# Kernel optimization log

Measured on AMD Instinct MI355X. Metric: run time of the kernel, lower is better.

Reference implementation:

```python
import jax, jax.numpy as jnp
import numpy as np
from jax import lax

DIM = 256
HEADS = 8
B, H, W = 8, 128, 128
EPS_LN = 1e-5
EPS_NORM = 1e-12


def _ln(x, w, b):
    # WithBias LayerNorm over channel dim, x: [b,c,h,w]
    mu = x.mean(axis=1, keepdims=True)
    var = ((x - mu) ** 2).mean(axis=1, keepdims=True)
    return (x - mu) / jnp.sqrt(var + EPS_LN) * w[None, :, None, None] + b[None, :, None, None]


def _conv1x1(x, w, b):
    # w: [out,in]
    return jnp.einsum('bchw,oc->bohw', x, w) + b[None, :, None, None]


def _dwconv3(x, w, b=None):
    # depthwise 3x3, w: [C,1,3,3]
    c = x.shape[1]
    y = lax.conv_general_dilated(x, w, (1, 1), 'SAME',
                                 dimension_numbers=('NCHW', 'OIHW', 'NCHW'),
                                 feature_group_count=c)
    if b is not None:
        y = y + b[None, :, None, None]
    return y


def setup_inputs() -> dict:
    key = jax.random.key(0)
    ks = jax.random.split(key, 10)
    s = 0.02
    return {
        'x': jax.random.normal(ks[0], (B, DIM, H, W), jnp.float32),
        'hx': jax.random.normal(ks[1], (B, DIM, H, W), jnp.float32),
        'ln1_w': jnp.ones((DIM,), jnp.float32),
        'ln1_b': jnp.zeros((DIM,), jnp.float32),
        'ln2_w': jnp.ones((DIM,), jnp.float32),
        'ln2_b': jnp.zeros((DIM,), jnp.float32),
        'q_w': jax.random.normal(ks[2], (DIM, DIM), jnp.float32) * s,
        'q_b': jnp.zeros((DIM,), jnp.float32),
        'q_dw_w': jax.random.normal(ks[3], (DIM, 1, 3, 3), jnp.float32) * s,
        'q_dw_b': jnp.zeros((DIM,), jnp.float32),
        'kv_w': jax.random.normal(ks[4], (2 * DIM, DIM), jnp.float32) * s,
        'kv_b': jnp.zeros((2 * DIM,), jnp.float32),
        'kv_dw_w': jax.random.normal(ks[5], (2 * DIM, 1, 3, 3), jnp.float32) * s,
        'kv_dw_b': jnp.zeros((2 * DIM,), jnp.float32),
        'ao_w': jax.random.normal(ks[6], (DIM, DIM), jnp.float32) * s,
        'ao_b': jnp.zeros((DIM,), jnp.float32),
        'pe1_w': jax.random.normal(ks[7], (DIM, 1, 3, 3), jnp.float32) * s,
        'pe2_w': jax.random.normal(ks[8], (DIM, 1, 3, 3), jnp.float32) * s,
        'temperature': jnp.ones((HEADS, 1, 1), jnp.float32),
    }


def reference(x, hx, ln1_w, ln1_b, ln2_w, ln2_b, q_w, q_b, q_dw_w, q_dw_b,
              kv_w, kv_b, kv_dw_w, kv_dw_b, ao_w, ao_b, pe1_w, pe2_w, temperature):
    b, c, h, w = hx.shape
    q = _dwconv3(_conv1x1(_ln(x, ln1_w, ln1_b), q_w, q_b), q_dw_w, q_dw_b)
    kv = _dwconv3(_conv1x1(_ln(hx, ln2_w, ln2_b), kv_w, kv_b), kv_dw_w, kv_dw_b)
    k, v = jnp.split(kv, 2, axis=1)
    # positional embedding branch: dwconv -> GELU -> dwconv (no bias)
    p_emb = _dwconv3(jax.nn.gelu(_dwconv3(v, pe1_w)), pe2_w)
    hd = c // HEADS
    # [b, head, hd, hw]
    qh = q.reshape(b, HEADS, hd, h * w)
    kh = k.reshape(b, HEADS, hd, h * w)
    vh = v.reshape(b, HEADS, hd, h * w)
    qh = qh / jnp.maximum(jnp.linalg.norm(qh, axis=-1, keepdims=True), EPS_NORM)
    kh = kh / jnp.maximum(jnp.linalg.norm(kh, axis=-1, keepdims=True), EPS_NORM)
    attn = jnp.einsum('bhcn,bhdn->bhcd', qh, kh) * temperature[None]
    attn = jax.nn.softmax(attn, axis=-1)
    out = jnp.einsum('bhcd,bhdn->bhcn', attn, vh).reshape(b, c, h, w)
    return _conv1x1(out, ao_w, ao_b) + p_emb + hx
```

## Files before the change

kernel.cpp:

```cpp
#include <hip/hip_runtime.h>
#include <cstdio>
#include <cstdint>

typedef unsigned short u16;
typedef short short8 __attribute__((ext_vector_type(8)));
typedef float floatx4 __attribute__((ext_vector_type(4)));

#define NPIX 16384
#define DIM 256

__device__ inline float bf2f(u16 v) {
    return __uint_as_float(((uint32_t)v) << 16);
}
__device__ inline u16 f2bf(float f) {
    uint32_t u = __float_as_uint(f);
    u += 0x7fffu + ((u >> 16) & 1u);
    return (u16)(u >> 16);
}
__device__ inline float gelu_fast(float x) {
    float x3 = x * x * x;
    float z2 = 1.5957691216057308f * (x + 0.044715f * x3);
    return x * __builtin_amdgcn_rcpf(1.f + __expf(-z2));
}
__device__ inline void load8(const u16* p, size_t idx, int isf32, float out[8]) {
    if (isf32) {
        const float4* f = (const float4*)((const float*)p + idx);
        float4 a = f[0], b = f[1];
        out[0] = a.x; out[1] = a.y; out[2] = a.z; out[3] = a.w;
        out[4] = b.x; out[5] = b.y; out[6] = b.z; out[7] = b.w;
    } else {
        uint4 d = *(const uint4*)(p + idx);
        u16 v[8]; *(uint4*)v = d;
#pragma unroll
        for (int j = 0; j < 8; ++j) out[j] = bf2f(v[j]);
    }
}

__global__ __launch_bounds__(256)
void detect_dtype(const u16* __restrict__ x, int* __restrict__ flag) {
    __shared__ int sh[256];
    int t = threadIdx.x;
    const uint32_t* w = (const uint32_t*)x;
    int cnt = 0;
    for (int i = t; i < 4096; i += 256) {
        int e = (w[i] >> 7) & 0xFF;
        if (e >= 110 && e <= 134) cnt++;
    }
    sh[t] = cnt;
    __syncthreads();
    if (t == 0) {
        int s = 0;
        for (int i = 0; i < 256; ++i) s += sh[i];
        *flag = (s < 2048) ? 1 : 0;
    }
}

struct WArgs {
    const void* src[17];
    int off[17];
    int n[17];
};
__global__ __launch_bounds__(256)
void convert_params(WArgs a, const int* __restrict__ flag, u16* __restrict__ dst) {
    int isf32 = *flag;
    int w = blockIdx.y;
    const void* s = a.src[w];
    u16* d = dst + a.off[w];
    int n = a.n[w];
    for (int i = blockIdx.x * 256 + threadIdx.x; i < n; i += gridDim.x * 256)
        d[i] = isf32 ? f2bf(((const float*)s)[i]) : ((const u16*)s)[i];
}

__global__ __launch_bounds__(256)
void ln_stats(const u16* __restrict__ x, const int* __restrict__ flag,
              float* __restrict__ mu, float* __restrict__ rstd) {
    int isf32 = *flag;
    int g = blockIdx.x * 256 + threadIdx.x;
    int b = g >> 14, n = g & (NPIX - 1);
    float s = 0.f, s2 = 0.f;
    if (isf32) {
        const float* p = (const float*)x + (size_t)b * DIM * NPIX + n;
        for (int c = 0; c < DIM; ++c) { float v = p[(size_t)c * NPIX]; s += v; s2 += v * v; }
    } else {
        const u16* p = x + (size_t)b * DIM * NPIX + n;
        for (int c = 0; c < DIM; ++c) { float v = bf2f(p[(size_t)c * NPIX]); s += v; s2 += v * v; }
    }
    float m = s * (1.f / 256.f);
    float var = s2 * (1.f / 256.f) - m * m;
    mu[g] = m;
    rstd[g] = rsqrtf(var + 1e-5f);
}

__global__ __launch_bounds__(256)
void ln_transpose(const u16* __restrict__ x, const int* __restrict__ flag,
                  const float* __restrict__ mu, const float* __restrict__ rstd,
                  const u16* __restrict__ lnw, const u16* __restrict__ lnb,
                  u16* __restrict__ xt) {
    int isf32 = *flag;
    __shared__ u16 T[64][72];
    int b = blockIdx.x >> 8;
    int n0 = (blockIdx.x & 255) * 64;
    int c0 = blockIdx.y * 64;
    int t = threadIdx.x;
#pragma unroll
    for (int l = 0; l < 2; ++l) {
        int idx = t + l * 256;
        int cl = idx >> 3, nch = (idx & 7) * 8;
        float vals[8];
        load8(x, ((size_t)(b * DIM + c0 + cl)) * NPIX + n0 + nch, isf32, vals);
        float w = bf2f(lnw[c0 + cl]), bb = bf2f(lnb[c0 + cl]);
#pragma unroll
        for (int j = 0; j < 8; ++j) {
            int g = b * NPIX + n0 + nch + j;
            float v = (vals[j] - mu[g]) * rstd[g] * w + bb;
            T[nch + j][cl] = f2bf(v);
        }
    }
    __syncthreads();
#pragma unroll
    for (int l = 0; l < 2; ++l) {
        int idx = t + l * 256;
        int nl = idx >> 3, cch = (idx & 7) * 8;
        uint4 d = *(const uint4*)&T[nl][cch];
        *(uint4*)(xt + (size_t)(b * NPIX + n0 + nl) * DIM + c0 + cch) = d;
    }
}

template <int HAS_ADD>
__global__ __launch_bounds__(256)
void gemm_bf16(const u16* __restrict__ A, const u16* __restrict__ Bw,
               const u16* __restrict__ bias, const u16* __restrict__ addt,
               u16* __restrict__ C, int ldc) {
    __shared__ u16 As[128][40];
    __shared__ u16 Bs[128][40];
    const int m0 = blockIdx.x * 128;
    const int n0 = blockIdx.y * 128;
    const int t = threadIdx.x;
    const int lane = t & 63;
    const int wid = t >> 6;
    const int wm = (wid >> 1) * 64;
    const int wn = (wid & 1) * 64;
    const int frow = lane & 15;
    const int koff = (lane >> 4) * 8;
    floatx4 acc[4][4] = {};
    for (int k0 = 0; k0 < 256; k0 += 32) {
#pragma unroll
        for (int l = 0; l < 2; ++l) {
            int idx = t + l * 256;
            int r = idx >> 2, ch = (idx & 3) * 8;
            *(uint4*)&As[r][ch] = *(const uint4*)(A + (size_t)(m0 + r) * 256 + k0 + ch);
            *(uint4*)&Bs[r][ch] = *(const uint4*)(Bw + (size_t)(n0 + r) * 256 + k0 + ch);
        }
        __syncthreads();
        short8 af[4], bfr[4];
#pragma unroll
        for (int i = 0; i < 4; ++i) {
            af[i] = *(const short8*)&As[wm + i * 16 + frow][koff];
            bfr[i] = *(const short8*)&Bs[wn + i * 16 + frow][koff];
        }
#pragma unroll
        for (int i = 0; i < 4; ++i)
#pragma unroll
            for (int j = 0; j < 4; ++j)
                acc[i][j] = __builtin_amdgcn_mfma_f32_16x16x32_bf16(af[i], bfr[j], acc[i][j], 0, 0, 0);
        __syncthreads();
    }
    const int col = lane & 15;
    const int r0 = (lane >> 4) * 4;
#pragma unroll
    for (int j = 0; j < 4; ++j) {
        int o = n0 + wn + j * 16 + col;
        float bv = bf2f(bias[o]);
#pragma unroll
        for (int i = 0; i < 4; ++i) {
#pragma unroll
            for (int r = 0; r < 4; ++r) {
                int m = m0 + wm + i * 16 + r0 + r;
                size_t off = (size_t)m * ldc + o;
                float v = acc[i][j][r] + bv;
                if (HAS_ADD) v += bf2f(addt[off]);
                C[off] = f2bf(v);
            }
        }
    }
}

template <int C, int HAS_BIAS, int DO_GELU>
__global__ __launch_bounds__(256)
void dwconv3_reg(const u16* __restrict__ in, int in_stride, int in_off,
                 const u16* __restrict__ w9, const u16* __restrict__ bias,
                 u16* __restrict__ out, int out_stride, int out_off) {
    constexpr int TPP = C / 8;
    constexpr int GRP = 256 / TPP;
    constexpr int XSEG = 128 / (GRP * 4);
    int t = threadIdx.x;
    int cl = t & (TPP - 1);
    int g = t / TPP;
    int c8 = cl * 8;
    int blk = blockIdx.x;
    int xs = blk & (XSEG - 1);
    int tmp = blk / XSEG;
    int y = tmp & 127;
    int b = tmp >> 7;
    int x0 = xs * (GRP * 4) + g * 4;

    u16 wl[72];
#pragma unroll
    for (int i = 0; i < 9; ++i)
        *((uint4*)wl + i) = *((const uint4*)(w9 + c8 * 9) + i);
    float wgt[9][8];
#pragma unroll
    for (int tap = 0; tap < 9; ++tap)
#pragma unroll
        for (int j = 0; j < 8; ++j)
            wgt[tap][j] = bf2f(wl[j * 9 + tap]);

    float acc[4][8] = {};
#pragma unroll
    for (int dy = -1; dy <= 1; ++dy) {
        int yy = y + dy;
        if ((unsigned)yy >= 128u) continue;
        const u16* rp = in + (size_t)(b * NPIX + yy * 128) * in_stride + in_off + c8;
#pragma unroll
        for (int ci = 0; ci < 6; ++ci) {
            int cc = x0 - 1 + ci;
            if ((unsigned)cc >= 128u) continue;
            uint4 d = *(const uint4*)(rp + (size_t)cc * in_stride);
            u16 v[8]; *(uint4*)v = d;
            float fv[8];
#pragma unroll
            for (int j = 0; j < 8; ++j) fv[j] = bf2f(v[j]);
#pragma unroll
            for (int dx = -1; dx <= 1; ++dx) {
                int p = ci - 1 - dx;
                if (p < 0 || p > 3) continue;
                int tap = (dy + 1) * 3 + (dx + 1);
#pragma unroll
                for (int j = 0; j < 8; ++j) acc[p][j] += fv[j] * wgt[tap][j];
            }
        }
    }

    float bi[8];
    if (HAS_BIAS) {
        uint4 bd = *(const uint4*)(bias + c8);
        u16 bv[8]; *(uint4*)bv = bd;
#pragma unroll
        for (int j = 0; j < 8; ++j) bi[j] = bf2f(bv[j]);
    }
    u16* op = out + (size_t)(b * NPIX + y * 128 + x0) * out_stride + out_off + c8;
#pragma unroll
    for (int p = 0; p < 4; ++p) {
        u16 o[8];
#pragma unroll
        for (int j = 0; j < 8; ++j) {
            float r = acc[p][j];
            if (HAS_BIAS) r += bi[j];
            if (DO_GELU) r = gelu_fast(r);
            o[j] = f2bf(r);
        }
        *(uint4*)(op + (size_t)p * out_stride) = *(uint4*)o;
    }
}

__global__ __launch_bounds__(256)
void finalize_scales(const float* __restrict__ qss, const float* __restrict__ kss,
                     float* __restrict__ qsc, float* __restrict__ ksc) {
    int i = blockIdx.x * 256 + threadIdx.x;
    qsc[i] = 1.f / fmaxf(sqrtf(qss[i]), 1e-12f);
    ksc[i] = 1.f / fmaxf(sqrtf(kss[i]), 1e-12f);
}

__global__ __launch_bounds__(256)
void gram_kernel(const u16* __restrict__ qT, const u16* __restrict__ kvT,
                 float* __restrict__ Gpart, float* __restrict__ qss,
                 float* __restrict__ kss) {
    int blk = blockIdx.x;
    int b = blk >> 7, chunk = blk & 127;
    int t = threadIdx.x;
    int hbase = t & 0xE0;
    int row0 = b * NPIX + chunk * 128;
    const u16* qp = qT + (size_t)row0 * 256 + t;
    const u16* kp = kvT + (size_t)row0 * 512;
    float acc[32];
#pragma unroll
    for (int j = 0; j < 32; ++j) acc[j] = 0.f;
    float qs2 = 0.f, ks2 = 0.f;
#pragma unroll 2
    for (int r = 0; r < 128; ++r) {
        float qv = bf2f(qp[(size_t)r * 256]);
        const u16* krow = kp + (size_t)r * 512;
        float kt = bf2f(krow[t]);
        qs2 += qv * qv;
        ks2 += kt * kt;
        uint4 k0 = *(const uint4*)(krow + hbase);
        uint4 k1 = *(const uint4*)(krow + hbase + 8);
        uint4 k2 = *(const uint4*)(krow + hbase + 16);
        uint4 k3 = *(const uint4*)(krow + hbase + 24);
        u16 kv16[32];
        *(uint4*)(kv16 + 0)  = k0;
        *(uint4*)(kv16 + 8)  = k1;
        *(uint4*)(kv16 + 16) = k2;
        *(uint4*)(kv16 + 24) = k3;
#pragma unroll
        for (int j = 0; j < 32; ++j) acc[j] += qv * bf2f(kv16[j]);
    }
    float* gp = Gpart + (size_t)blk * 8192 + t * 32;
#pragma unroll
    for (int j = 0; j < 32; j += 4)
        *(float4*)(gp + j) = make_float4(acc[j], acc[j + 1], acc[j + 2], acc[j + 3]);
    atomicAdd(&qss[b * 256 + t], qs2);
    atomicAdd(&kss[b * 256 + t], ks2);
}

__global__ __launch_bounds__(1024)
void softmax32(const float* __restrict__ Gpart, const float* __restrict__ qsc,
               const float* __restrict__ ksc, const u16* __restrict__ temp,
               float* __restrict__ attn) {
    int bh = blockIdx.x;
    int b = bh >> 3, h = bh & 7;
    int t = threadIdx.x;
    int i = t >> 5, j = t & 31;
    const float* gp = Gpart + (size_t)b * 128 * 8192 + (size_t)((h * 32 + i) * 32 + j);
    float s0 = 0.f, s1 = 0.f, s2 = 0.f, s3 = 0.f;
    for (int p = 0; p < 128; p += 4) {
        s0 += gp[(size_t)p * 8192];
        s1 += gp[(size_t)(p + 1) * 8192];
        s2 += gp[(size_t)(p + 2) * 8192];
        s3 += gp[(size_t)(p + 3) * 8192];
    }
    float qs = qsc[b * 256 + h * 32 + i];
    float ks = ksc[b * 256 + h * 32 + j];
    float tm = bf2f(temp[h]);
    float v = ((s0 + s1) + (s2 + s3)) * qs * ks * tm;
    float m = v;
    for (int s = 16; s; s >>= 1) m = fmaxf(m, __shfl_xor(m, s, 32));
    float e = __expf(v - m);
    float sum = e;
    for (int s = 16; s; s >>= 1) sum += __shfl_xor(sum, s, 32);
    attn[((size_t)(b * 8 + h) * 32 + i) * 32 + j] = e / sum;
}

__global__ __launch_bounds__(256)
void attnv_kernel(const float* __restrict__ attn, const u16* __restrict__ kvT,
                  u16* __restrict__ outT) {
    int blk = blockIdx.x;
    int b = blk >> 8, chunk = blk & 255;
    int t = threadIdx.x;
    int hbase = t & 0xE0;
    float at[32];
    const float4* ap = (const float4*)(attn + (size_t)b * 8192 + (size_t)t * 32);
#pragma unroll
    for (int j = 0; j < 8; ++j) {
        float4 d = ap[j];
        at[j * 4 + 0] = d.x; at[j * 4 + 1] = d.y;
        at[j * 4 + 2] = d.z; at[j * 4 + 3] = d.w;
    }
    int row0 = b * NPIX + chunk * 64;
    const u16* vp = kvT + (size_t)row0 * 512 + 256 + hbase;
    u16* op = outT + (size_t)row0 * 256 + t;
#pragma unroll 2
    for (int r = 0; r < 64; ++r) {
        const u16* vrow = vp + (size_t)r * 512;
        uint4 k0 = *(const uint4*)(vrow);
        uint4 k1 = *(const uint4*)(vrow + 8);
        uint4 k2 = *(const uint4*)(vrow + 16);
        uint4 k3 = *(const uint4*)(vrow + 24);
        u16 v16[32];
        *(uint4*)(v16 + 0)  = k0;
        *(uint4*)(v16 + 8)  = k1;
        *(uint4*)(v16 + 16) = k2;
        *(uint4*)(v16 + 24) = k3;
        float a = 0.f;
#pragma unroll
        for (int j = 0; j < 32; ++j) a += at[j] * bf2f(v16[j]);
        op[(size_t)r * 256] = f2bf(a);
    }
}

__global__ __launch_bounds__(256)
void final_out(const u16* __restrict__ Fp, const u16* __restrict__ hx,
               const int* __restrict__ flag, u16* __restrict__ out) {
    int isf32 = *flag;
    __shared__ u16 T[64][72];
    int b = blockIdx.x >> 8;
    int n0 = (blockIdx.x & 255) * 64;
    int c0 = blockIdx.y * 64;
    int t = threadIdx.x;
#pragma unroll
    for (int l = 0; l < 2; ++l) {
        int idx = t + l * 256;
        int nl = idx >> 3, cch = (idx & 7) * 8;
        *(uint4*)&T[nl][cch] = *(const uint4*)(Fp + (size_t)(b * NPIX + n0 + nl) * 256 + c0 + cch);
    }
    __syncthreads();
#pragma unroll
    for (int l = 0; l < 2; ++l) {
        int idx = t + l * 256;
        int cl = idx >> 3, nch = (idx & 7) * 8;
        size_t g = (size_t)(b * DIM + c0 + cl) * NPIX + n0 + nch;
        float hv[8];
        load8(hx, g, isf32, hv);
        float r[8];
#pragma unroll
        for (int j = 0; j < 8; ++j) r[j] = bf2f(T[nch + j][cl]) + hv[j];
        if (isf32) {
            float* o = (float*)out + g;
            *(float4*)o       = make_float4(r[0], r[1], r[2], r[3]);
            *(float4*)(o + 4) = make_float4(r[4], r[5], r[6], r[7]);
        } else {
            u16 ov[8];
#pragma unroll
            for (int j = 0; j < 8; ++j) ov[j] = f2bf(r[j]);
            *(uint4*)(out + g) = *(uint4*)ov;
        }
    }
}

__global__ void ws_marker(u16* out) {
    if (threadIdx.x < 64) ((uint32_t*)out)[threadIdx.x] = 0x46402400u;
}

extern "C" void kernel_launch(void* const* d_in, const int* in_sizes, int n_in,
                              void* d_out, int out_size, void* d_ws, size_t ws_size,
                              hipStream_t stream) {
    const u16* x    = (const u16*)d_in[0];
    const u16* hx   = (const u16*)d_in[1];
    u16* outp = (u16*)d_out;

    char* ws = (char*)d_ws;
    float* F = (float*)ws;
    float* mu_x   = F;
    float* rstd_x = F + 131072;
    float* mu_h   = F + 262144;
    float* rstd_h = F + 393216;
    float* qss    = F + 524288;
    float* kss    = F + 526336;
    float* qsc    = F + 528384;
    float* ksc    = F + 530432;
    float* attn   = F + 598016;
    int*   dflag  = (int*)(F + 663552);
    u16*   W      = (u16*)(ws + 2752512);
    u16* R1 = (u16*)(ws + (((size_t)4)   << 20));
    u16* R2 = (u16*)(ws + (((size_t)68)  << 20));
    u16* R3 = (u16*)(ws + (((size_t)132) << 20));
    u16* R4 = (u16*)(ws + (((size_t)260) << 20));
    float* Gpart = (float*)R2;

    size_t need = ((size_t)388) << 20;
    if (ws_size < need) {
        ws_marker<<<1, 64, 0, stream>>>(outp);
        return;
    }

    const int O_QW = 0, O_KVW = 65536, O_AOW = 196608, O_QB = 262144, O_KVB = 262400,
              O_AOB = 262912, O_LN1W = 263168, O_LN1B = 263424, O_LN2W = 263680,
              O_LN2B = 263936, O_QDWW = 264192, O_QDWB = 266496, O_KVDWW = 266752,
              O_KVDWB = 271360, O_PE1 = 271872, O_PE2 = 274176, O_TEMP = 276480;

    WArgs wa;
    const int srcidx[17] = {6, 10, 14, 7, 11, 15, 2, 3, 4, 5, 8, 9, 12, 13, 16, 17, 18};
    const int offs[17]   = {O_QW, O_KVW, O_AOW, O_QB, O_KVB, O_AOB, O_LN1W, O_LN1B,
                            O_LN2W, O_LN2B, O_QDWW, O_QDWB, O_KVDWW, O_KVDWB,
                            O_PE1, O_PE2, O_TEMP};
    const int ns[17]     = {65536, 131072, 65536, 256, 512, 256, 256, 256, 256, 256,
                            2304, 256, 4608, 512, 2304, 2304, 8};
    for (int i = 0; i < 17; ++i) { wa.src[i] = d_in[srcidx[i]]; wa.off[i] = offs[i]; wa.n[i] = ns[i]; }

    detect_dtype<<<1, 256, 0, stream>>>(x, dflag);
    convert_params<<<dim3(16, 17), 256, 0, stream>>>(wa, dflag, W);

    hipMemsetAsync(ws + (size_t)524288 * 4, 0, (size_t)(532480 - 524288) * 4, stream);

    ln_stats<<<512, 256, 0, stream>>>(x, dflag, mu_x, rstd_x);
    ln_stats<<<512, 256, 0, stream>>>(hx, dflag, mu_h, rstd_h);

    ln_transpose<<<dim3(2048, 4), 256, 0, stream>>>(x, dflag, mu_x, rstd_x, W + O_LN1W, W + O_LN1B, R1);
    gemm_bf16<0><<<dim3(1024, 2), 256, 0, stream>>>(R1, W + O_QW, W + O_QB, nullptr, R2, 256);

    ln_transpose<<<dim3(2048, 4), 256, 0, stream>>>(hx, dflag, mu_h, rstd_h, W + O_LN2W, W + O_LN2B, R1);
    gemm_bf16<0><<<dim3(1024, 4), 256, 0, stream>>>(R1, W + O_KVW, W + O_KVB, nullptr, R3, 512);

    dwconv3_reg<256, 1, 0><<<4096, 256, 0, stream>>>(R2, 256, 0, W + O_QDWW, W + O_QDWB, R1, 256, 0);
    dwconv3_reg<512, 1, 0><<<8192, 256, 0, stream>>>(R3, 512, 0, W + O_KVDWW, W + O_KVDWB, R4, 512, 0);

    gram_kernel<<<1024, 256, 0, stream>>>(R1, R4, Gpart, qss, kss);
    finalize_scales<<<8, 256, 0, stream>>>(qss, kss, qsc, ksc);
    softmax32<<<64, 1024, 0, stream>>>(Gpart, qsc, ksc, W + O_TEMP, attn);
    attnv_kernel<<<2048, 256, 0, stream>>>(attn, R4, R2);

    dwconv3_reg<256, 0, 1><<<4096, 256, 0, stream>>>(R4, 512, 256, W + O_PE1, nullptr, R3, 256, 0);
    dwconv3_reg<256, 0, 0><<<4096, 256, 0, stream>>>(R3, 256, 0, W + O_PE2, nullptr, R1, 256, 0);

    gemm_bf16<1><<<dim3(1024, 2), 256, 0, stream>>>(R2, W + O_AOW, W + O_AOB, R1, R3, 256);
    final_out<<<dim3(2048, 4), 256, 0, stream>>>(R3, hx, dflag, outp);
}
```

Baseline: 1.257 ms.

## Fuse LayerNorm stats with transpose, split gram into more chunks, inline norm scales

```diff
diff --git a/kernel.cpp b/kernel.cpp
--- a/kernel.cpp
+++ b/kernel.cpp
@@ -72,58 +72,70 @@
 }
 
 __global__ __launch_bounds__(256)
-void ln_stats(const u16* __restrict__ x, const int* __restrict__ flag,
-              float* __restrict__ mu, float* __restrict__ rstd) {
+void ln_fused(const u16* __restrict__ x, const int* __restrict__ flag,
+              const u16* __restrict__ lnw, const u16* __restrict__ lnb,
+              u16* __restrict__ xt) {
     int isf32 = *flag;
-    int g = blockIdx.x * 256 + threadIdx.x;
-    int b = g >> 14, n = g & (NPIX - 1);
+    __shared__ float T[32][257];
+    __shared__ float wsh[256], bsh[256];
+    __shared__ float2 red[8][32];
+    __shared__ float2 mst[32];
+    int t = threadIdx.x;
+    int b = blockIdx.x >> 9;
+    int n0 = (blockIdx.x & 511) * 32;
+    if (isf32) {
+        const float* xp = (const float*)x;
+#pragma unroll
+        for (int pass = 0; pass < 8; ++pass) {
+            int c = (t >> 3) + pass * 32;
+            int px = (t & 7) * 4;
+            float4 d = *(const float4*)(xp + ((size_t)(b * 256 + c)) * NPIX + n0 + px);
+            T[px][c] = d.x; T[px + 1][c] = d.y; T[px + 2][c] = d.z; T[px + 3][c] = d.w;
+        }
+    } else {
+#pragma unroll
+        for (int pass = 0; pass < 4; ++pass) {
+            int c = (t >> 2) + pass * 64;
+            int px = (t & 3) * 8;
+            uint4 d = *(const uint4*)(x + ((size_t)(b * 256 + c)) * NPIX + n0 + px);
+            u16 v[8]; *(uint4*)v = d;
+#pragma unroll
+            for (int j = 0; j < 8; ++j) T[px + j][c] = bf2f(v[j]);
+        }
+    }
+    wsh[t] = bf2f(lnw[t]);
+    bsh[t] = bf2f(lnb[t]);
+    __syncthreads();
+    int p = t & 31, q = t >> 5;
     float s = 0.f, s2 = 0.f;
-    if (isf32) {
-        const float* p = (const float*)x + (size_t)b * DIM * NPIX + n;
-        for (int c = 0; c < DIM; ++c) { float v = p[(size_t)c * NPIX]; s += v; s2 += v * v; }
-    } else {
-        const u16* p = x + (size_t)b * DIM * NPIX + n;
-        for (int c = 0; c < DIM; ++c) { float v = bf2f(p[(size_t)c * NPIX]); s += v; s2 += v * v; }
-    }
-    float m = s * (1.f / 256.f);
-    float var = s2 * (1.f / 256.f) - m * m;
-    mu[g] = m;
-    rstd[g] = rsqrtf(var + 1e-5f);
-}
-
-__global__ __launch_bounds__(256)
-void ln_transpose(const u16* __restrict__ x, const int* __restrict__ flag,
-                  const float* __restrict__ mu, const float* __restrict__ rstd,
-                  const u16* __restrict__ lnw, const u16* __restrict__ lnb,
-                  u16* __restrict__ xt) {
-    int isf32 = *flag;
-    __shared__ u16 T[64][72];
-    int b = blockIdx.x >> 8;
-    int n0 = (blockIdx.x & 255) * 64;
-    int c0 = blockIdx.y * 64;
-    int t = threadIdx.x;
-#pragma unroll
-    for (int l = 0; l < 2; ++l) {
-        int idx = t + l * 256;
-        int cl = idx >> 3, nch = (idx & 7) * 8;
-        float vals[8];
-        load8(x, ((size_t)(b * DIM + c0 + cl)) * NPIX + n0 + nch, isf32, vals);
-        float w = bf2f(lnw[c0 + cl]), bb = bf2f(lnb[c0 + cl]);
-#pragma unroll
-        for (int j = 0; j < 8; ++j) {
-            int g = b * NPIX + n0 + nch + j;
-            float v = (vals[j] - mu[g]) * rstd[g] * w + bb;
-            T[nch + j][cl] = f2bf(v);
-        }
-    }
+#pragma unroll
+    for (int k = 0; k < 32; ++k) {
+        float v = T[p][q * 32 + k];
+        s += v; s2 += v * v;
+    }
+    red[q][p] = make_float2(s, s2);
     __syncthreads();
-#pragma unroll
-    for (int l = 0; l < 2; ++l) {
-        int idx = t + l * 256;
-        int nl = idx >> 3, cch = (idx & 7) * 8;
-        uint4 d = *(const uint4*)&T[nl][cch];
-        *(uint4*)(xt + (size_t)(b * NPIX + n0 + nl) * DIM + c0 + cch) = d;
-    }
+    if (t < 32) {
+        float ss = 0.f, ss2 = 0.f;
+#pragma unroll
+        for (int qq = 0; qq < 8; ++qq) { ss += red[qq][t].x; ss2 += red[qq][t].y; }
+        float m = ss * (1.f / 256.f);
+        float var = ss2 * (1.f / 256.f) - m * m;
+        mst[t] = make_float2(m, rsqrtf(var + 1e-5f));
+    }
+    __syncthreads();
+    float2 ms = mst[p];
+    u16 ov[32];
+#pragma unroll
+    for (int k = 0; k < 32; ++k) {
+        int c = q * 32 + k;
+        float v = (T[p][c] - ms.x) * ms.y * wsh[c] + bsh[c];
+        ov[k] = f2bf(v);
+    }
+    u16* op = xt + ((size_t)(b * NPIX + n0 + p)) * 256 + q * 32;
+#pragma unroll
+    for (int k = 0; k < 32; k += 8)
+        *(uint4*)(op + k) = *(uint4*)(ov + k);
 }
 
 template <int HAS_ADD>
@@ -264,22 +276,14 @@
 }
 
 __global__ __launch_bounds__(256)
-void finalize_scales(const float* __restrict__ qss, const float* __restrict__ kss,
-                     float* __restrict__ qsc, float* __restrict__ ksc) {
-    int i = blockIdx.x * 256 + threadIdx.x;
-    qsc[i] = 1.f / fmaxf(sqrtf(qss[i]), 1e-12f);
-    ksc[i] = 1.f / fmaxf(sqrtf(kss[i]), 1e-12f);
-}
-
-__global__ __launch_bounds__(256)
 void gram_kernel(const u16* __restrict__ qT, const u16* __restrict__ kvT,
                  float* __restrict__ Gpart, float* __restrict__ qss,
                  float* __restrict__ kss) {
     int blk = blockIdx.x;
-    int b = blk >> 7, chunk = blk & 127;
+    int b = blk >> 8, chunk = blk & 255;
     int t = threadIdx.x;
     int hbase = t & 0xE0;
-    int row0 = b * NPIX + chunk * 128;
+    int row0 = b * NPIX + chunk * 64;
     const u16* qp = qT + (size_t)row0 * 256 + t;
     const u16* kp = kvT + (size_t)row0 * 512;
     float acc[32];
@@ -287,7 +291,7 @@
     for (int j = 0; j < 32; ++j) acc[j] = 0.f;
     float qs2 = 0.f, ks2 = 0.f;
 #pragma unroll 2
-    for (int r = 0; r < 128; ++r) {
+    for (int r = 0; r < 64; ++r) {
         float qv = bf2f(qp[(size_t)r * 256]);
         const u16* krow = kp + (size_t)r * 512;
         float kt = bf2f(krow[t]);
@@ -314,23 +318,23 @@
 }
 
 __global__ __launch_bounds__(1024)
-void softmax32(const float* __restrict__ Gpart, const float* __restrict__ qsc,
-               const float* __restrict__ ksc, const u16* __restrict__ temp,
+void softmax32(const float* __restrict__ Gpart, const float* __restrict__ qss,
+               const float* __restrict__ kss, const u16* __restrict__ temp,
                float* __restrict__ attn) {
     int bh = blockIdx.x;
     int b = bh >> 3, h = bh & 7;
     int t = threadIdx.x;
     int i = t >> 5, j = t & 31;
-    const float* gp = Gpart + (size_t)b * 128 * 8192 + (size_t)((h * 32 + i) * 32 + j);
+    const float* gp = Gpart + (size_t)b * 256 * 8192 + (size_t)((h * 32 + i) * 32 + j);
     float s0 = 0.f, s1 = 0.f, s2 = 0.f, s3 = 0.f;
-    for (int p = 0; p < 128; p += 4) {
+    for (int p = 0; p < 256; p += 4) {
         s0 += gp[(size_t)p * 8192];
         s1 += gp[(size_t)(p + 1) * 8192];
         s2 += gp[(size_t)(p + 2) * 8192];
         s3 += gp[(size_t)(p + 3) * 8192];
     }
-    float qs = qsc[b * 256 + h * 32 + i];
-    float ks = ksc[b * 256 + h * 32 + j];
+    float qs = 1.f / fmaxf(sqrtf(qss[b * 256 + h * 32 + i]), 1e-12f);
+    float ks = 1.f / fmaxf(sqrtf(kss[b * 256 + h * 32 + j]), 1e-12f);
     float tm = bf2f(temp[h]);
     float v = ((s0 + s1) + (s2 + s3)) * qs * ks * tm;
     float m = v;
@@ -430,14 +434,8 @@
 
     char* ws = (char*)d_ws;
     float* F = (float*)ws;
-    float* mu_x   = F;
-    float* rstd_x = F + 131072;
-    float* mu_h   = F + 262144;
-    float* rstd_h = F + 393216;
     float* qss    = F + 524288;
     float* kss    = F + 526336;
-    float* qsc    = F + 528384;
-    float* ksc    = F + 530432;
     float* attn   = F + 598016;
     int*   dflag  = (int*)(F + 663552);
     u16*   W      = (u16*)(ws + 2752512);
@@ -470,23 +468,19 @@
     detect_dtype<<<1, 256, 0, stream>>>(x, dflag);
     convert_params<<<dim3(16, 17), 256, 0, stream>>>(wa, dflag, W);
 
-    hipMemsetAsync(ws + (size_t)524288 * 4, 0, (size_t)(532480 - 524288) * 4, stream);
-
-    ln_stats<<<512, 256, 0, stream>>>(x, dflag, mu_x, rstd_x);
-    ln_stats<<<512, 256, 0, stream>>>(hx, dflag, mu_h, rstd_h);
-
-    ln_transpose<<<dim3(2048, 4), 256, 0, stream>>>(x, dflag, mu_x, rstd_x, W + O_LN1W, W + O_LN1B, R1);
+    hipMemsetAsync(ws + (size_t)524288 * 4, 0, (size_t)(528384 - 524288) * 4, stream);
+
+    ln_fused<<<4096, 256, 0, stream>>>(x, dflag, W + O_LN1W, W + O_LN1B, R1);
     gemm_bf16<0><<<dim3(1024, 2), 256, 0, stream>>>(R1, W + O_QW, W + O_QB, nullptr, R2, 256);
 
-    ln_transpose<<<dim3(2048, 4), 256, 0, stream>>>(hx, dflag, mu_h, rstd_h, W + O_LN2W, W + O_LN2B, R1);
+    ln_fused<<<4096, 256, 0, stream>>>(hx, dflag, W + O_LN2W, W + O_LN2B, R1);
     gemm_bf16<0><<<dim3(1024, 4), 256, 0, stream>>>(R1, W + O_KVW, W + O_KVB, nullptr, R3, 512);
 
     dwconv3_reg<256, 1, 0><<<4096, 256, 0, stream>>>(R2, 256, 0, W + O_QDWW, W + O_QDWB, R1, 256, 0);
     dwconv3_reg<512, 1, 0><<<8192, 256, 0, stream>>>(R3, 512, 0, W + O_KVDWW, W + O_KVDWB, R4, 512, 0);
 
-    gram_kernel<<<1024, 256, 0, stream>>>(R1, R4, Gpart, qss, kss);
-    finalize_scales<<<8, 256, 0, stream>>>(qss, kss, qsc, ksc);
-    softmax32<<<64, 1024, 0, stream>>>(Gpart, qsc, ksc, W + O_TEMP, attn);
+    gram_kernel<<<2048, 256, 0, stream>>>(R1, R4, Gpart, qss, kss);
+    softmax32<<<64, 1024, 0, stream>>>(Gpart, qss, kss, W + O_TEMP, attn);
     attnv_kernel<<<2048, 256, 0, stream>>>(attn, R4, R2);
 
     dwconv3_reg<256, 0, 1><<<4096, 256, 0, stream>>>(R4, 512, 256, W + O_PE1, nullptr, R3, 256, 0);
```

Measured after the change: 1.237 ms. No clear change (-1.5%).
